# Kernel optimization log

Hardware: AMD Instinct MI355X
Metric: run time of the kernel (lower is better)

Reference implementation:

```python
import jax, jax.numpy as jnp
import numpy as np

HEADS = 4
DIM_HEAD = 4


def setup_inputs() -> dict:
    key = jax.random.key(0)
    k1, k2, k3, k4 = jax.random.split(key, 4)
    B, C, H, W = 4, 64, 64, 64
    hidden = HEADS * DIM_HEAD  # 16
    x = jax.random.normal(k1, (B, C, H, W), dtype=jnp.float32)
    # 1x1 convs are just channel matmuls; store squeezed kernels
    w_qkv = jax.random.normal(k2, (3 * hidden, C), dtype=jnp.float32) * 0.05
    w_out = jax.random.normal(k3, (C, hidden), dtype=jnp.float32) * 0.05
    b_out = jax.random.normal(k4, (C,), dtype=jnp.float32) * 0.05
    return {"x": x, "w_qkv": w_qkv, "w_out": w_out, "b_out": b_out}


def reference(x, w_qkv, w_out, b_out):
    B, C, H, W = x.shape
    n = H * W
    scale = DIM_HEAD ** -0.5
    # to_qkv: 1x1 conv, no bias -> [B, 3*hidden, n]
    qkv = jnp.einsum('oc,bcn->bon', w_qkv, x.reshape(B, C, n))
    q, k, v = jnp.split(qkv, 3, axis=1)
    # 'b (h d) n -> b h d n'
    def to_heads(t):
        return t.reshape(B, HEADS, DIM_HEAD, n)
    q, k, v = to_heads(q) * scale, to_heads(k), to_heads(v)
    sim = jnp.einsum('bhdi,bhdj->bhij', q, k)           # [B,H,n,n]
    attn = jax.nn.softmax(sim, axis=-1)
    out = jnp.einsum('bhij,bhdj->bhid', attn, v)        # [B,H,n,d]
    # 'b h n d -> b (h d) h w'
    out = out.transpose(0, 1, 3, 2).reshape(B, HEADS * DIM_HEAD, H, W)
    # to_out: 1x1 conv with bias
    y = jnp.einsum('oc,bchw->bohw', w_out, out) + b_out[None, :, None, None]
    return y
```

## Files before the change

kernel.cpp:

```cpp
#include <hip/hip_runtime.h>
#include <hip/hip_bf16.h>

#define N_POS 4096
#define BH 16
#define JS 4

typedef float f32x16 __attribute__((ext_vector_type(16)));
typedef short bf16x8 __attribute__((ext_vector_type(8)));

#define QSCALE (0.5f * 1.44269504088896f)

__device__ __forceinline__ float fexp2(float x) {
#if __has_builtin(__builtin_amdgcn_exp2f)
    return __builtin_amdgcn_exp2f(x);
#else
    return exp2f(x);
#endif
}

__device__ __forceinline__ unsigned int bfbits(float f) {
    __hip_bfloat16 h = __float2bfloat16(f);
    return (unsigned int)*reinterpret_cast<unsigned short*>(&h);
}
__device__ __forceinline__ float bff32(unsigned int u) {
    unsigned int w = u << 16;
    float f;
    __builtin_memcpy(&f, &w, 4);
    return f;
}
__device__ __forceinline__ unsigned int pk2(unsigned int lo, unsigned int hi) {
    return lo | (hi << 16);
}

__global__ __launch_bounds__(256) void qkv_pack(const float* __restrict__ x,
                                                const float* __restrict__ w_qkv,
                                                uint4* __restrict__ qfrag,
                                                uint4* __restrict__ kfrag,
                                                unsigned short* __restrict__ vfrag) {
    int blk = blockIdx.x;
    int chunk = blk & 15;
    int bh = blk >> 4;
    int b = bh >> 2, h = bh & 3;
    int i = chunk * 256 + threadIdx.x;

    const float* xb = x + ((size_t)b * 64) * N_POS + i;
    const float* wq = w_qkv + (h * 4) * 64;
    const float* wk = w_qkv + (16 + h * 4) * 64;
    const float* wv = w_qkv + (32 + h * 4) * 64;

    float aq[4] = {0, 0, 0, 0}, ak[4] = {0, 0, 0, 0}, av[4] = {0, 0, 0, 0};
#pragma unroll 8
    for (int c = 0; c < 64; ++c) {
        float xv = xb[(size_t)c * N_POS];
#pragma unroll
        for (int d = 0; d < 4; ++d) {
            aq[d] = fmaf(wq[d * 64 + c], xv, aq[d]);
            ak[d] = fmaf(wk[d * 64 + c], xv, ak[d]);
            av[d] = fmaf(wv[d * 64 + c], xv, av[d]);
        }
    }

    unsigned int qh[4], ql[4], kh[4], kl[4];
#pragma unroll
    for (int d = 0; d < 4; ++d) {
        float qs = aq[d] * QSCALE;
        qh[d] = bfbits(qs);
        ql[d] = bfbits(qs - bff32(qh[d]));
        kh[d] = bfbits(ak[d]);
        kl[d] = bfbits(ak[d] - bff32(kh[d]));
    }

    int it = i >> 5, il = i & 31;
    size_t base = ((size_t)(bh * 128 + it) * 2) * 32 + il;
    qfrag[base]      = make_uint4(pk2(qh[0], qh[1]), pk2(qh[2], qh[3]),
                                  pk2(ql[0], ql[1]), pk2(ql[2], ql[3]));
    qfrag[base + 32] = make_uint4(pk2(qh[0], qh[1]), pk2(qh[2], qh[3]), 0u, 0u);
    kfrag[base]      = make_uint4(pk2(kh[0], kh[1]), pk2(kh[2], kh[3]),
                                  pk2(kh[0], kh[1]), pk2(kh[2], kh[3]));
    kfrag[base + 32] = make_uint4(pk2(kl[0], kl[1]), pk2(kl[2], kl[3]), 0u, 0u);

    int step = i >> 4, vh = (i >> 3) & 1, e = i & 7;
    size_t ventry = ((size_t)(bh * 256 + step) * 2 + vh) * 5;
#pragma unroll
    for (int d = 0; d < 4; ++d)
        vfrag[(ventry + d) * 8 + e] = (unsigned short)bfbits(av[d]);
    if (e == 0)
        reinterpret_cast<uint4*>(vfrag)[ventry + 4] =
            make_uint4(0x3F803F80u, 0x3F803F80u, 0x3F803F80u, 0x3F803F80u);
}

__global__ __launch_bounds__(256, 4) void attn_mfma(const uint4* __restrict__ qfrag,
                                                    const uint4* __restrict__ kfrag,
                                                    const uint4* __restrict__ vfrag,
                                                    float* __restrict__ pacc,
                                                    float* __restrict__ pl) {
    constexpr int JT = 128 / JS;
    int wave = threadIdx.x >> 6;
    int lane = threadIdx.x & 63;
    int half = lane >> 5, c = lane & 31;
    int blk = blockIdx.x;
    int js = blk & (JS - 1);
    int itg = (blk >> 2) & 31;
    int bh = blk >> 7;
    int it = itg * 4 + wave;

    uint4 qf_u = qfrag[((size_t)(bh * 128 + it) * 2 + half) * 32 + c];
    bf16x8 qf = __builtin_bit_cast(bf16x8, qf_u);

    const uint4* kp = kfrag + (size_t)bh * 128 * 64 + (size_t)js * JT * 64
                    + (size_t)half * 32 + c;
    int vcol = c < 4 ? c : 4;
    const uint4* vp = vfrag + (size_t)bh * 2560 + (size_t)js * JT * 20
                    + half * 5 + vcol;

    f32x16 acc, zc;
#pragma unroll
    for (int r = 0; r < 16; ++r) { acc[r] = 0.f; zc[r] = 0.f; }

    uint4 kf_c = kp[0];
    uint4 v0_c = vp[0];
    uint4 v1_c = vp[10];

#pragma unroll 2
    for (int jj = 0; jj < JT; ++jj) {
        int jn = (jj + 1) & (JT - 1);
        uint4 kf_n = kp[jn * 64];
        uint4 v0_n = vp[(2 * jn) * 10];
        uint4 v1_n = vp[(2 * jn + 1) * 10];

        bf16x8 kf = __builtin_bit_cast(bf16x8, kf_c);
        f32x16 s = __builtin_amdgcn_mfma_f32_32x32x16_bf16(kf, qf, zc, 0, 0, 0);
        unsigned int t[8];
#pragma unroll
        for (int eo = 0; eo < 8; ++eo) {
            float plo = fexp2(s[2 * eo]);
            float phi = fexp2(s[2 * eo + 1]);
            unsigned int r_;
            asm("v_cvt_pk_bf16_f32 %0, %1, %2" : "=v"(r_) : "v"(plo), "v"(phi));
            t[eo] = r_;
        }
        asm("v_permlane32_swap_b32 %0, %1" : "+v"(t[0]), "+v"(t[2]));
        asm("v_permlane32_swap_b32 %0, %1" : "+v"(t[1]), "+v"(t[3]));
        asm("v_permlane32_swap_b32 %0, %1" : "+v"(t[4]), "+v"(t[6]));
        asm("v_permlane32_swap_b32 %0, %1" : "+v"(t[5]), "+v"(t[7]));
        bf16x8 pa0 = __builtin_bit_cast(bf16x8, make_uint4(t[0], t[1], t[2], t[3]));
        bf16x8 pa1 = __builtin_bit_cast(bf16x8, make_uint4(t[4], t[5], t[6], t[7]));
        bf16x8 v0 = __builtin_bit_cast(bf16x8, v0_c);
        bf16x8 v1 = __builtin_bit_cast(bf16x8, v1_c);
        acc = __builtin_amdgcn_mfma_f32_32x32x16_bf16(pa0, v0, acc, 0, 0, 0);
        acc = __builtin_amdgcn_mfma_f32_32x32x16_bf16(pa1, v1, acc, 0, 0, 0);

        kf_c = kf_n; v0_c = v0_n; v1_c = v1_n;
    }

    size_t pbase = (size_t)(js * BH + bh) * N_POS + it * 32;
    if (c < 4) {
#pragma unroll
        for (int r = 0; r < 16; ++r) {
            int row = (r & 3) + 8 * (r >> 2) + 4 * half;
            pacc[(pbase + row) * 4 + c] = acc[r];
        }
    } else if (c == 4) {
#pragma unroll
        for (int r = 0; r < 16; ++r) {
            int row = (r & 3) + 8 * (r >> 2) + 4 * half;
            pl[pbase + row] = acc[r];
        }
    }
}

__global__ __launch_bounds__(256) void out_proj(const float4* __restrict__ pacc,
                                                const float* __restrict__ pl,
                                                const float* __restrict__ w_out,
                                                const float* __restrict__ b_out,
                                                float* __restrict__ y) {
    int t = blockIdx.x * 256 + threadIdx.x;
    int b  = t >> 14;
    int cq = (t >> 12) & 3;
    int i  = t & 4095;

    float of[16];
#pragma unroll
    for (int h = 0; h < 4; ++h) {
        int bh = b * 4 + h;
        float sx = 0.f, sy = 0.f, sz = 0.f, sw = 0.f, l = 0.f;
#pragma unroll
        for (int js = 0; js < JS; ++js) {
            size_t idx = (size_t)(js * BH + bh) * N_POS + i;
            float4 a = pacc[idx];
            sx += a.x; sy += a.y; sz += a.z; sw += a.w;
            l += pl[idx];
        }
        float inv = 1.0f / l;
        of[h * 4 + 0] = sx * inv;
        of[h * 4 + 1] = sy * inv;
        of[h * 4 + 2] = sz * inv;
        of[h * 4 + 3] = sw * inv;
    }

    float* yb = y + ((size_t)b * 64 + cq * 16) * N_POS + i;
#pragma unroll
    for (int cc = 0; cc < 16; ++cc) {
        const float* wr = w_out + (cq * 16 + cc) * 16;
        float s = b_out[cq * 16 + cc];
#pragma unroll
        for (int u = 0; u < 16; ++u) s = fmaf(wr[u], of[u], s);
        yb[(size_t)cc * N_POS] = s;
    }
}

extern "C" void kernel_launch(void* const* d_in, const int* in_sizes, int n_in,
                              void* d_out, int out_size, void* d_ws, size_t ws_size,
                              hipStream_t stream) {
    const float* x     = (const float*)d_in[0];
    const float* w_qkv = (const float*)d_in[1];
    const float* w_out = (const float*)d_in[2];
    const float* b_out = (const float*)d_in[3];
    float* y = (float*)d_out;

    char* w = (char*)d_ws;
    uint4*          qfrag = (uint4*)(w);
    uint4*          kfrag = (uint4*)(w + 2097152);
    unsigned short* vfrag = (unsigned short*)(w + 4194304);
    float*          pacc  = (float*)(w + 5242880);
    float*          pl    = (float*)(w + 5242880 + (size_t)JS * 1048576);

    qkv_pack<<<256, 256, 0, stream>>>(x, w_qkv, qfrag, kfrag, vfrag);
    attn_mfma<<<BH * 32 * JS, 256, 0, stream>>>(qfrag, kfrag, (const uint4*)vfrag,
                                                pacc, pl);
    out_proj<<<256, 256, 0, stream>>>((const float4*)pacc, pl, w_out, b_out, y);
}
```

Baseline: 54.53 us.

## Split QKV/out-proj across more blocks, dual accumulators, partial polynomial exp2

The QKV projection kernel now launches three times as many blocks, each computing only Q, K or V, and the output projection launches four times as many blocks, each producing 4 output channels. Both raise parallelism for these small kernels, at the cost of recomputing the head reduction and rereading x across blocks. In the attention loop, the two P·V MFMAs now accumulate into separate registers to break the dependency chain. Three of the eight exp2 pairs use a polynomial on the VALU instead of the transcendental unit, to spread the exp work across units.

```diff
diff --git a/kernel.cpp b/kernel.cpp
--- a/kernel.cpp
+++ b/kernel.cpp
@@ -18,6 +18,18 @@
 #endif
 }
 
+__device__ __forceinline__ float poly_exp2(float x) {
+    float n = rintf(x);
+    float f = x - n;
+    float p = fmaf(f, fmaf(f, fmaf(f, fmaf(f, fmaf(f,
+                  0.00133336f, 0.00961813f), 0.05550411f), 0.24022651f),
+                  0.69314718f), 1.0f);
+    unsigned int bits = (unsigned int)((int)n + 127) << 23;
+    float scale;
+    __builtin_memcpy(&scale, &bits, 4);
+    return p * scale;
+}
+
 __device__ __forceinline__ unsigned int bfbits(float f) {
     __hip_bfloat16 h = __float2bfloat16(f);
     return (unsigned int)*reinterpret_cast<unsigned short*>(&h);
@@ -38,55 +50,58 @@
                                                 uint4* __restrict__ kfrag,
                                                 unsigned short* __restrict__ vfrag) {
     int blk = blockIdx.x;
+    int role = blk >> 8;
+    int bh = (blk >> 4) & 15;
     int chunk = blk & 15;
-    int bh = blk >> 4;
     int b = bh >> 2, h = bh & 3;
     int i = chunk * 256 + threadIdx.x;
 
     const float* xb = x + ((size_t)b * 64) * N_POS + i;
-    const float* wq = w_qkv + (h * 4) * 64;
-    const float* wk = w_qkv + (16 + h * 4) * 64;
-    const float* wv = w_qkv + (32 + h * 4) * 64;
-
-    float aq[4] = {0, 0, 0, 0}, ak[4] = {0, 0, 0, 0}, av[4] = {0, 0, 0, 0};
+    const float* wr = w_qkv + (role * 16 + h * 4) * 64;
+
+    float a[4] = {0, 0, 0, 0};
 #pragma unroll 8
     for (int c = 0; c < 64; ++c) {
         float xv = xb[(size_t)c * N_POS];
 #pragma unroll
-        for (int d = 0; d < 4; ++d) {
-            aq[d] = fmaf(wq[d * 64 + c], xv, aq[d]);
-            ak[d] = fmaf(wk[d * 64 + c], xv, ak[d]);
-            av[d] = fmaf(wv[d * 64 + c], xv, av[d]);
-        }
-    }
-
-    unsigned int qh[4], ql[4], kh[4], kl[4];
-#pragma unroll
-    for (int d = 0; d < 4; ++d) {
-        float qs = aq[d] * QSCALE;
-        qh[d] = bfbits(qs);
-        ql[d] = bfbits(qs - bff32(qh[d]));
-        kh[d] = bfbits(ak[d]);
-        kl[d] = bfbits(ak[d] - bff32(kh[d]));
+        for (int d = 0; d < 4; ++d)
+            a[d] = fmaf(wr[d * 64 + c], xv, a[d]);
     }
 
     int it = i >> 5, il = i & 31;
     size_t base = ((size_t)(bh * 128 + it) * 2) * 32 + il;
-    qfrag[base]      = make_uint4(pk2(qh[0], qh[1]), pk2(qh[2], qh[3]),
-                                  pk2(ql[0], ql[1]), pk2(ql[2], ql[3]));
-    qfrag[base + 32] = make_uint4(pk2(qh[0], qh[1]), pk2(qh[2], qh[3]), 0u, 0u);
-    kfrag[base]      = make_uint4(pk2(kh[0], kh[1]), pk2(kh[2], kh[3]),
-                                  pk2(kh[0], kh[1]), pk2(kh[2], kh[3]));
-    kfrag[base + 32] = make_uint4(pk2(kl[0], kl[1]), pk2(kl[2], kl[3]), 0u, 0u);
-
-    int step = i >> 4, vh = (i >> 3) & 1, e = i & 7;
-    size_t ventry = ((size_t)(bh * 256 + step) * 2 + vh) * 5;
-#pragma unroll
-    for (int d = 0; d < 4; ++d)
-        vfrag[(ventry + d) * 8 + e] = (unsigned short)bfbits(av[d]);
-    if (e == 0)
-        reinterpret_cast<uint4*>(vfrag)[ventry + 4] =
-            make_uint4(0x3F803F80u, 0x3F803F80u, 0x3F803F80u, 0x3F803F80u);
+
+    if (role == 0) {
+        unsigned int qh[4], ql[4];
+#pragma unroll
+        for (int d = 0; d < 4; ++d) {
+            float qs = a[d] * QSCALE;
+            qh[d] = bfbits(qs);
+            ql[d] = bfbits(qs - bff32(qh[d]));
+        }
+        qfrag[base]      = make_uint4(pk2(qh[0], qh[1]), pk2(qh[2], qh[3]),
+                                      pk2(ql[0], ql[1]), pk2(ql[2], ql[3]));
+        qfrag[base + 32] = make_uint4(pk2(qh[0], qh[1]), pk2(qh[2], qh[3]), 0u, 0u);
+    } else if (role == 1) {
+        unsigned int kh[4], kl[4];
+#pragma unroll
+        for (int d = 0; d < 4; ++d) {
+            kh[d] = bfbits(a[d]);
+            kl[d] = bfbits(a[d] - bff32(kh[d]));
+        }
+        kfrag[base]      = make_uint4(pk2(kh[0], kh[1]), pk2(kh[2], kh[3]),
+                                      pk2(kh[0], kh[1]), pk2(kh[2], kh[3]));
+        kfrag[base + 32] = make_uint4(pk2(kl[0], kl[1]), pk2(kl[2], kl[3]), 0u, 0u);
+    } else {
+        int step = i >> 4, vh = (i >> 3) & 1, e = i & 7;
+        size_t ventry = ((size_t)(bh * 256 + step) * 2 + vh) * 5;
+#pragma unroll
+        for (int d = 0; d < 4; ++d)
+            vfrag[(ventry + d) * 8 + e] = (unsigned short)bfbits(a[d]);
+        if (e == 0)
+            reinterpret_cast<uint4*>(vfrag)[ventry + 4] =
+                make_uint4(0x3F803F80u, 0x3F803F80u, 0x3F803F80u, 0x3F803F80u);
+    }
 }
 
 __global__ __launch_bounds__(256, 4) void attn_mfma(const uint4* __restrict__ qfrag,
@@ -113,9 +128,9 @@
     const uint4* vp = vfrag + (size_t)bh * 2560 + (size_t)js * JT * 20
                     + half * 5 + vcol;
 
-    f32x16 acc, zc;
-#pragma unroll
-    for (int r = 0; r < 16; ++r) { acc[r] = 0.f; zc[r] = 0.f; }
+    f32x16 acc0, acc1, zc;
+#pragma unroll
+    for (int r = 0; r < 16; ++r) { acc0[r] = 0.f; acc1[r] = 0.f; zc[r] = 0.f; }
 
     uint4 kf_c = kp[0];
     uint4 v0_c = vp[0];
@@ -133,8 +148,14 @@
         unsigned int t[8];
 #pragma unroll
         for (int eo = 0; eo < 8; ++eo) {
-            float plo = fexp2(s[2 * eo]);
-            float phi = fexp2(s[2 * eo + 1]);
+            float plo, phi;
+            if (eo < 5) {
+                plo = fexp2(s[2 * eo]);
+                phi = fexp2(s[2 * eo + 1]);
+            } else {
+                plo = poly_exp2(s[2 * eo]);
+                phi = poly_exp2(s[2 * eo + 1]);
+            }
             unsigned int r_;
             asm("v_cvt_pk_bf16_f32 %0, %1, %2" : "=v"(r_) : "v"(plo), "v"(phi));
             t[eo] = r_;
@@ -147,8 +168,8 @@
         bf16x8 pa1 = __builtin_bit_cast(bf16x8, make_uint4(t[4], t[5], t[6], t[7]));
         bf16x8 v0 = __builtin_bit_cast(bf16x8, v0_c);
         bf16x8 v1 = __builtin_bit_cast(bf16x8, v1_c);
-        acc = __builtin_amdgcn_mfma_f32_32x32x16_bf16(pa0, v0, acc, 0, 0, 0);
-        acc = __builtin_amdgcn_mfma_f32_32x32x16_bf16(pa1, v1, acc, 0, 0, 0);
+        acc0 = __builtin_amdgcn_mfma_f32_32x32x16_bf16(pa0, v0, acc0, 0, 0, 0);
+        acc1 = __builtin_amdgcn_mfma_f32_32x32x16_bf16(pa1, v1, acc1, 0, 0, 0);
 
         kf_c = kf_n; v0_c = v0_n; v1_c = v1_n;
     }
@@ -158,13 +179,13 @@
 #pragma unroll
         for (int r = 0; r < 16; ++r) {
             int row = (r & 3) + 8 * (r >> 2) + 4 * half;
-            pacc[(pbase + row) * 4 + c] = acc[r];
+            pacc[(pbase + row) * 4 + c] = acc0[r] + acc1[r];
         }
     } else if (c == 4) {
 #pragma unroll
         for (int r = 0; r < 16; ++r) {
             int row = (r & 3) + 8 * (r >> 2) + 4 * half;
-            pl[pbase + row] = acc[r];
+            pl[pbase + row] = acc0[r] + acc1[r];
         }
     }
 }
@@ -175,9 +196,9 @@
                                                 const float* __restrict__ b_out,
                                                 float* __restrict__ y) {
     int t = blockIdx.x * 256 + threadIdx.x;
-    int b  = t >> 14;
-    int cq = (t >> 12) & 3;
     int i  = t & 4095;
+    int cg = (t >> 12) & 15;
+    int b  = t >> 16;
 
     float of[16];
 #pragma unroll
@@ -198,11 +219,12 @@
         of[h * 4 + 3] = sw * inv;
     }
 
-    float* yb = y + ((size_t)b * 64 + cq * 16) * N_POS + i;
-#pragma unroll
-    for (int cc = 0; cc < 16; ++cc) {
-        const float* wr = w_out + (cq * 16 + cc) * 16;
-        float s = b_out[cq * 16 + cc];
+    float* yb = y + ((size_t)b * 64 + cg * 4) * N_POS + i;
+#pragma unroll
+    for (int cc = 0; cc < 4; ++cc) {
+        int ch = cg * 4 + cc;
+        const float* wr = w_out + ch * 16;
+        float s = b_out[ch];
 #pragma unroll
         for (int u = 0; u < 16; ++u) s = fmaf(wr[u], of[u], s);
         yb[(size_t)cc * N_POS] = s;
@@ -225,8 +247,8 @@
     float*          pacc  = (float*)(w + 5242880);
     float*          pl    = (float*)(w + 5242880 + (size_t)JS * 1048576);
 
-    qkv_pack<<<256, 256, 0, stream>>>(x, w_qkv, qfrag, kfrag, vfrag);
+    qkv_pack<<<3 * 256, 256, 0, stream>>>(x, w_qkv, qfrag, kfrag, vfrag);
     attn_mfma<<<BH * 32 * JS, 256, 0, stream>>>(qfrag, kfrag, (const uint4*)vfrag,
                                                 pacc, pl);
-    out_proj<<<256, 256, 0, stream>>>((const float4*)pacc, pl, w_out, b_out, y);
-}
+    out_proj<<<1024, 256, 0, stream>>>((const float4*)pacc, pl, w_out, b_out, y);
+}
```

Measured after the change: 71.58 us. 1.31x slower.
